# Kernel tuning notes

Measured on AMD Instinct MI355X. Metric: run time of the kernel, lower is better.

## Reference

```python
import jax, jax.numpy as jnp
import numpy as np

NEG_INF = -1e9


def setup_inputs() -> dict:
    key0 = jax.random.key(0)
    ks = jax.random.split(key0, 7)
    B, Tq, Tv, D, U = 8, 512, 512, 512, 128
    query = jax.random.normal(ks[0], (B, Tq, D), dtype=jnp.float32)
    key = jax.random.normal(ks[1], (B, Tv, D), dtype=jnp.float32)
    value = jax.random.normal(ks[2], (B, Tv, D), dtype=jnp.float32)
    mask = jax.random.randint(ks[3], (B, Tv), 0, 2).astype(bool)
    mask = mask.at[:, 0].set(True)  # ensure no fully-masked row
    Wa = jax.random.normal(ks[4], (D, U), dtype=jnp.float32) * (1.0 / np.sqrt(D))
    Ua = jax.random.normal(ks[5], (D, U), dtype=jnp.float32) * (1.0 / np.sqrt(D))
    scale = jax.random.normal(ks[6], (U,), dtype=jnp.float32) * 0.1
    return {"query": query, "key": key, "value": value, "mask": mask,
            "Wa": Wa, "Ua": Ua, "scale": scale}


def reference(query, key, value, mask, Wa, Ua, scale):
    # Dense projections (no bias)
    q = query @ Wa          # [B, Tq, U]
    k = key @ Ua            # [B, Tv, U]
    # Additive (Bahdanau) scores with learned per-unit scale:
    # scores[b,i,j] = sum_u scale[u] * tanh(q[b,i,u] + k[b,j,u])
    t = jnp.tanh(q[:, :, None, :] + k[:, None, :, :])   # [B, Tq, Tv, U]
    scores = jnp.einsum('bijU,U->bij', t, scale)         # [B, Tq, Tv]
    # Mask padded keys/values then softmax over Tv
    scores = jnp.where(mask[:, None, :], scores, NEG_INF)
    weights = jax.nn.softmax(scores, axis=-1)            # [B, Tq, Tv]
    # Weighted sum of values (query_mask is all-True in source -> no-op)
    context = jnp.einsum('bij,bjd->bid', weights, value) # [B, Tq, D]
    return context
```

## Files before the change

### kernel.cpp

```cpp
#include <hip/hip_runtime.h>

constexpr int Bb = 8;
constexpr int Tq = 512;
constexpr int Tv = 512;
constexpr int Dd = 512;
constexpr int Uu = 128;
constexpr float C2LOG2E = 2.88539008177792681f;
constexpr float LOG2E   = 1.44269504088896341f;

__global__ __launch_bounds__(256, 4) void proj_kernel(
    const float* __restrict__ query,
    const float* __restrict__ key,
    const float* __restrict__ Wa,
    const float* __restrict__ Ua,
    const int* __restrict__ mask,
    float* __restrict__ qf2, float* __restrict__ kT)
{
    const int R    = blockIdx.x * 8;
    const bool isQ = R < Bb * Tq;
    const float* __restrict__ src = isQ ? query : key;
    const float* __restrict__ W   = isQ ? Wa : Ua;
    const int Rloc = isQ ? R : R - Bb * Tq;

    __shared__ float x[8 * Dd];
    __shared__ int posLoc[8];
    const int t = threadIdx.x;

    {
        const float4* __restrict__ s4 =
            reinterpret_cast<const float4*>(src + (size_t)Rloc * Dd);
        float4* x4 = reinterpret_cast<float4*>(x);
#pragma unroll
        for (int m = 0; m < 4; ++m) x4[t + 256 * m] = s4[t + 256 * m];
    }
    if (!isQ && t < 64) {
        const int b  = Rloc >> 9;
        const int j0 = Rloc & 511;
        int base = 0;
#pragma unroll
        for (int c = 0; c < 8; ++c) {
            const int j = c * 64 + t;
            const int v = (mask[b * 512 + j] != 0);
            const unsigned long long bits = __ballot(v);
            const int pos = base + (int)__popcll(bits & ((1ull << t) - 1ull));
            if (j >= j0 && j < j0 + 8) posLoc[j - j0] = v ? pos : -1;
            base += (int)__popcll(bits);
        }
    }
    __syncthreads();

    const int ub = t & 63;
    const int dq = t >> 6;
    const float* __restrict__ Wq = W + (size_t)dq * 128 * Uu;
    const float* __restrict__ xq = x + dq * 128;

    float acc[8][2];
#pragma unroll
    for (int r = 0; r < 8; ++r) { acc[r][0] = 0.f; acc[r][1] = 0.f; }

#pragma unroll 2
    for (int d4 = 0; d4 < 32; ++d4) {
        const int d = d4 * 4;
        const float w0x = Wq[(d + 0) * Uu + ub], w1x = Wq[(d + 0) * Uu + ub + 64];
        const float w0y = Wq[(d + 1) * Uu + ub], w1y = Wq[(d + 1) * Uu + ub + 64];
        const float w0z = Wq[(d + 2) * Uu + ub], w1z = Wq[(d + 2) * Uu + ub + 64];
        const float w0w = Wq[(d + 3) * Uu + ub], w1w = Wq[(d + 3) * Uu + ub + 64];
#pragma unroll
        for (int r = 0; r < 8; ++r) {
            const float4 xv = *reinterpret_cast<const float4*>(xq + r * Dd + d);
            acc[r][0] = fmaf(xv.x, w0x, acc[r][0]);
            acc[r][0] = fmaf(xv.y, w0y, acc[r][0]);
            acc[r][0] = fmaf(xv.z, w0z, acc[r][0]);
            acc[r][0] = fmaf(xv.w, w0w, acc[r][0]);
            acc[r][1] = fmaf(xv.x, w1x, acc[r][1]);
            acc[r][1] = fmaf(xv.y, w1y, acc[r][1]);
            acc[r][1] = fmaf(xv.z, w1z, acc[r][1]);
            acc[r][1] = fmaf(xv.w, w1w, acc[r][1]);
        }
    }

    __syncthreads();
    {
        float* __restrict__ part = x;
#pragma unroll
        for (int r = 0; r < 8; ++r) {
            part[(dq * 8 + r) * 128 + ub]      = acc[r][0];
            part[(dq * 8 + r) * 128 + ub + 64] = acc[r][1];
        }
    }
    __syncthreads();

    {
        const float* __restrict__ part = x;
        const int r  = t >> 5;
        const int u0 = (t & 31) * 4;
        const float4 p0 = *reinterpret_cast<const float4*>(part + (0 * 8 + r) * 128 + u0);
        const float4 p1 = *reinterpret_cast<const float4*>(part + (1 * 8 + r) * 128 + u0);
        const float4 p2 = *reinterpret_cast<const float4*>(part + (2 * 8 + r) * 128 + u0);
        const float4 p3 = *reinterpret_cast<const float4*>(part + (3 * 8 + r) * 128 + u0);
        float4 v;
        v.x = C2LOG2E * (p0.x + p1.x + p2.x + p3.x);
        v.y = C2LOG2E * (p0.y + p1.y + p2.y + p3.y);
        v.z = C2LOG2E * (p0.z + p1.z + p2.z + p3.z);
        v.w = C2LOG2E * (p0.w + p1.w + p2.w + p3.w);
        if (isQ) {
            *reinterpret_cast<float4*>(qf2 + (size_t)(Rloc + r) * Uu + u0) = v;
        } else {
            const int p = posLoc[r];
            if (p >= 0) {
                float* __restrict__ kb = kT + (size_t)(Rloc >> 9) * Uu * Tv;
                const int u4a = u0 >> 2;
                *reinterpret_cast<float4*>(kb + ((size_t)u4a * Tv + p) * 4) = v;
            }
        }
    }
}

__global__ __launch_bounds__(512, 8) void attn_kernel(
    const float* __restrict__ qf2, const float* __restrict__ kT,
    const float* __restrict__ value,
    const int* __restrict__ mask,
    const float* __restrict__ scale,
    float* __restrict__ out)
{
    const int bid = blockIdx.x;
    const int swz = (bid & 7) * 128 + (bid >> 3);
    const int r0 = swz * 4;
    const int b  = r0 >> 9;
    const int t  = threadIdx.x;

    __shared__ float q2[4 * Uu];
    __shared__ float s2[Uu];
    __shared__ int   jl[Tv];
    __shared__ float w[4 * Tv];
    __shared__ float pbuf[4 * Tv];
    __shared__ float inv4[4];
    __shared__ int   cntS;

    jl[t] = 0;
    if (t < 128)
        reinterpret_cast<float4*>(q2)[t] =
            reinterpret_cast<const float4*>(qf2 + (size_t)r0 * Uu)[t];
    else if (t < 256) s2[t - 128] = scale[t - 128];
    __syncthreads();
    if (t < 64) {
        int base = 0;
#pragma unroll
        for (int c = 0; c < 8; ++c) {
            const int j = c * 64 + t;
            const int v = (mask[b * 512 + j] != 0);
            const unsigned long long bits = __ballot(v);
            const int pos = base + (int)__popcll(bits & ((1ull << t) - 1ull));
            if (v) jl[pos] = j;
            base += (int)__popcll(bits);
        }
        if (t == 0) cntS = base;
    }
    __syncthreads();

    const int cnt   = cntS;
    const int cntp4 = (cnt + 3) & ~3;

    {
        const int g   = t >> 8;
        const int jc0 = t & 255;
        const float4* __restrict__ kb4 =
            reinterpret_cast<const float4*>(kT) + (size_t)b * 32 * Tv + (size_t)g * 16 * Tv;
        float* __restrict__ wr = g ? pbuf : w;
        for (int jb = 0; jb < cnt; jb += 256) {
            const int jc = jb + jc0;
            if (jc < cnt) {
                float acc[4] = {0, 0, 0, 0};
#pragma unroll 2
                for (int u4 = 0; u4 < 16; ++u4) {
                    const float4 kv = kb4[(size_t)u4 * Tv + jc];
                    const float4 sv = reinterpret_cast<const float4*>(s2)[g * 16 + u4];
#pragma unroll
                    for (int i = 0; i < 4; ++i) {
                        const float4 qv = *reinterpret_cast<const float4*>(
                            q2 + i * Uu + (g * 16 + u4) * 4);
                        float e0 = __builtin_amdgcn_exp2f(qv.x + kv.x);
                        float e1 = __builtin_amdgcn_exp2f(qv.y + kv.y);
                        float e2 = __builtin_amdgcn_exp2f(qv.z + kv.z);
                        float e3 = __builtin_amdgcn_exp2f(qv.w + kv.w);
                        acc[i] = fmaf(sv.x, __builtin_amdgcn_rcpf(e0 + 1.f), acc[i]);
                        acc[i] = fmaf(sv.y, __builtin_amdgcn_rcpf(e1 + 1.f), acc[i]);
                        acc[i] = fmaf(sv.z, __builtin_amdgcn_rcpf(e2 + 1.f), acc[i]);
                        acc[i] = fmaf(sv.w, __builtin_amdgcn_rcpf(e3 + 1.f), acc[i]);
                    }
                }
#pragma unroll
                for (int i = 0; i < 4; ++i) wr[i * Tv + jc] = acc[i];
            }
        }
    }
    __syncthreads();

    {
        const int wv = t >> 6, ln = t & 63;
        if (wv < 4) {
            float* __restrict__ row        = w    + wv * Tv;
            const float* __restrict__ rowB = pbuf + wv * Tv;
            float vals[8];
            float m = -3e38f;
#pragma unroll
            for (int c = 0; c < 8; ++c) {
                const int e = ln + 64 * c;
                vals[c] = (e < cnt) ? -2.f * (row[e] + rowB[e]) : -3e38f;
                m = fmaxf(m, vals[c]);
            }
#pragma unroll
            for (int off = 32; off; off >>= 1) m = fmaxf(m, __shfl_xor(m, off, 64));
            float sum = 0.f;
#pragma unroll
            for (int c = 0; c < 8; ++c) {
                const int e = ln + 64 * c;
                if (e < cnt) {
                    float ex = __builtin_amdgcn_exp2f((vals[c] - m) * LOG2E);
                    row[e] = ex;
                    sum += ex;
                } else {
                    row[e] = 0.f;
                }
            }
#pragma unroll
            for (int off = 32; off; off >>= 1) sum += __shfl_xor(sum, off, 64);
            if (ln == 0) inv4[wv] = 1.0f / sum;
        }
    }
    __syncthreads();

    const int mid = ((cntp4 >> 1) + 3) & ~3;
    const int g  = t >> 8;
    const int c  = t & 255;
    const int d0 = c * 2;
    const int jbeg = g ? mid : 0;
    const int jend = g ? cntp4 : mid;
    const float* __restrict__ vb = value + (size_t)b * Tv * Dd + d0;
    float ax[4], ay[4];
#pragma unroll
    for (int i = 0; i < 4; ++i) { ax[i] = 0.f; ay[i] = 0.f; }

    for (int jj = jbeg; jj < jend; jj += 4) {
        const int4 rows = *reinterpret_cast<const int4*>(jl + jj);
        const float2 v0 = *reinterpret_cast<const float2*>(vb + (size_t)rows.x * Dd);
        const float2 v1 = *reinterpret_cast<const float2*>(vb + (size_t)rows.y * Dd);
        const float2 v2 = *reinterpret_cast<const float2*>(vb + (size_t)rows.z * Dd);
        const float2 v3 = *reinterpret_cast<const float2*>(vb + (size_t)rows.w * Dd);
#pragma unroll
        for (int i = 0; i < 4; ++i) {
            const float4 wq = *reinterpret_cast<const float4*>(w + i * Tv + jj);
            ax[i] = fmaf(wq.x, v0.x, ax[i]); ay[i] = fmaf(wq.x, v0.y, ay[i]);
            ax[i] = fmaf(wq.y, v1.x, ax[i]); ay[i] = fmaf(wq.y, v1.y, ay[i]);
            ax[i] = fmaf(wq.z, v2.x, ax[i]); ay[i] = fmaf(wq.z, v2.y, ay[i]);
            ax[i] = fmaf(wq.w, v3.x, ax[i]); ay[i] = fmaf(wq.w, v3.y, ay[i]);
        }
    }

    if (g == 1) {
#pragma unroll
        for (int i = 0; i < 4; ++i) {
            float2 p; p.x = ax[i]; p.y = ay[i];
            *reinterpret_cast<float2*>(pbuf + i * Dd + d0) = p;
        }
    }
    __syncthreads();
    if (g == 0) {
#pragma unroll
        for (int i = 0; i < 4; ++i) {
            const float inv = inv4[i];
            const float2 p1 = *reinterpret_cast<const float2*>(pbuf + i * Dd + d0);
            float2 o;
            o.x = (ax[i] + p1.x) * inv;
            o.y = (ay[i] + p1.y) * inv;
            *reinterpret_cast<float2*>(out + (size_t)(r0 + i) * Dd + d0) = o;
        }
    }
}

extern "C" void kernel_launch(void* const* d_in, const int* in_sizes, int n_in,
                              void* d_out, int out_size, void* d_ws, size_t ws_size,
                              hipStream_t stream)
{
    const float* query = (const float*)d_in[0];
    const float* key   = (const float*)d_in[1];
    const float* value = (const float*)d_in[2];
    const int*   mask  = (const int*)d_in[3];
    const float* Wa    = (const float*)d_in[4];
    const float* Ua    = (const float*)d_in[5];
    const float* scale = (const float*)d_in[6];
    float* out = (float*)d_out;

    float* qf2 = (float*)d_ws;
    float* kT  = qf2 + Bb * Tq * Uu;

    proj_kernel<<<(2 * Bb * Tq) / 8, 256, 0, stream>>>(query, key, Wa, Ua, mask, qf2, kT);
    attn_kernel<<<(Bb * Tq) / 4, 512, 0, stream>>>(qf2, kT, value, mask, scale, out);
}
```

Before: 153.5 us.

## Precompute exponentials in projection so attention uses product instead of exp

The projection kernel now stores exp2(2*log2e*q) and exp2(2*log2e*k) instead of the scaled projections. The attention inner loop then forms 1 + eq*ek with one FMA in place of an exp2 of a sum, cutting a transcendental from the hot Tv*U*Tq loop. The projection is also reorganised to 512 threads, each covering 64 of the D dimensions, with an 8-way partial reduction. Risk: exp of large projections can overflow to inf or lose precision, though rcp(inf) still gives 0 so tanh saturation stays correct.

Measured after the change: 151.2 us. Within noise of the previous version (-1.5%).

```diff
diff --git a/kernel.cpp b/kernel.cpp
--- a/kernel.cpp
+++ b/kernel.cpp
@@ -8,7 +8,7 @@
 constexpr float C2LOG2E = 2.88539008177792681f;
 constexpr float LOG2E   = 1.44269504088896341f;
 
-__global__ __launch_bounds__(256, 4) void proj_kernel(
+__global__ __launch_bounds__(512, 8) void proj_kernel(
     const float* __restrict__ query,
     const float* __restrict__ key,
     const float* __restrict__ Wa,
@@ -22,8 +22,9 @@
     const float* __restrict__ W   = isQ ? Wa : Ua;
     const int Rloc = isQ ? R : R - Bb * Tq;
 
-    __shared__ float x[8 * Dd];
+    __shared__ float smem[8 * 8 * 128];
     __shared__ int posLoc[8];
+    float* __restrict__ x = smem;
     const int t = threadIdx.x;
 
     {
@@ -31,7 +32,7 @@
             reinterpret_cast<const float4*>(src + (size_t)Rloc * Dd);
         float4* x4 = reinterpret_cast<float4*>(x);
 #pragma unroll
-        for (int m = 0; m < 4; ++m) x4[t + 256 * m] = s4[t + 256 * m];
+        for (int m = 0; m < 2; ++m) x4[t + 512 * m] = s4[t + 512 * m];
     }
     if (!isQ && t < 64) {
         const int b  = Rloc >> 9;
@@ -51,15 +52,15 @@
 
     const int ub = t & 63;
     const int dq = t >> 6;
-    const float* __restrict__ Wq = W + (size_t)dq * 128 * Uu;
-    const float* __restrict__ xq = x + dq * 128;
+    const float* __restrict__ Wq = W + (size_t)dq * 64 * Uu;
+    const float* __restrict__ xq = x + dq * 64;
 
     float acc[8][2];
 #pragma unroll
     for (int r = 0; r < 8; ++r) { acc[r][0] = 0.f; acc[r][1] = 0.f; }
 
 #pragma unroll 2
-    for (int d4 = 0; d4 < 32; ++d4) {
+    for (int d4 = 0; d4 < 16; ++d4) {
         const int d = d4 * 4;
         const float w0x = Wq[(d + 0) * Uu + ub], w1x = Wq[(d + 0) * Uu + ub + 64];
         const float w0y = Wq[(d + 1) * Uu + ub], w1y = Wq[(d + 1) * Uu + ub + 64];
@@ -81,7 +82,7 @@
 
     __syncthreads();
     {
-        float* __restrict__ part = x;
+        float* __restrict__ part = smem;
 #pragma unroll
         for (int r = 0; r < 8; ++r) {
             part[(dq * 8 + r) * 128 + ub]      = acc[r][0];
@@ -91,26 +92,28 @@
     __syncthreads();
 
     {
-        const float* __restrict__ part = x;
-        const int r  = t >> 5;
-        const int u0 = (t & 31) * 4;
-        const float4 p0 = *reinterpret_cast<const float4*>(part + (0 * 8 + r) * 128 + u0);
-        const float4 p1 = *reinterpret_cast<const float4*>(part + (1 * 8 + r) * 128 + u0);
-        const float4 p2 = *reinterpret_cast<const float4*>(part + (2 * 8 + r) * 128 + u0);
-        const float4 p3 = *reinterpret_cast<const float4*>(part + (3 * 8 + r) * 128 + u0);
-        float4 v;
-        v.x = C2LOG2E * (p0.x + p1.x + p2.x + p3.x);
-        v.y = C2LOG2E * (p0.y + p1.y + p2.y + p3.y);
-        v.z = C2LOG2E * (p0.z + p1.z + p2.z + p3.z);
-        v.w = C2LOG2E * (p0.w + p1.w + p2.w + p3.w);
+        const float* __restrict__ part = smem;
+        const int r  = t >> 6;
+        const int u0 = (t & 63) * 2;
+        float s0 = 0.f, s1 = 0.f;
+#pragma unroll
+        for (int p = 0; p < 8; ++p) {
+            const float2 pv = *reinterpret_cast<const float2*>(part + (p * 8 + r) * 128 + u0);
+            s0 += pv.x;
+            s1 += pv.y;
+        }
+        float2 e;
+        e.x = __builtin_amdgcn_exp2f(C2LOG2E * s0);
+        e.y = __builtin_amdgcn_exp2f(C2LOG2E * s1);
         if (isQ) {
-            *reinterpret_cast<float4*>(qf2 + (size_t)(Rloc + r) * Uu + u0) = v;
+            *reinterpret_cast<float2*>(qf2 + (size_t)(Rloc + r) * Uu + u0) = e;
         } else {
             const int p = posLoc[r];
             if (p >= 0) {
                 float* __restrict__ kb = kT + (size_t)(Rloc >> 9) * Uu * Tv;
-                const int u4a = u0 >> 2;
-                *reinterpret_cast<float4*>(kb + ((size_t)u4a * Tv + p) * 4) = v;
+                const int u4 = u0 >> 2;
+                const int c  = u0 & 3;
+                *reinterpret_cast<float2*>(kb + ((size_t)u4 * Tv + p) * 4 + c) = e;
             }
         }
     }
@@ -179,14 +182,14 @@
                     for (int i = 0; i < 4; ++i) {
                         const float4 qv = *reinterpret_cast<const float4*>(
                             q2 + i * Uu + (g * 16 + u4) * 4);
-                        float e0 = __builtin_amdgcn_exp2f(qv.x + kv.x);
-                        float e1 = __builtin_amdgcn_exp2f(qv.y + kv.y);
-                        float e2 = __builtin_amdgcn_exp2f(qv.z + kv.z);
-                        float e3 = __builtin_amdgcn_exp2f(qv.w + kv.w);
-                        acc[i] = fmaf(sv.x, __builtin_amdgcn_rcpf(e0 + 1.f), acc[i]);
-                        acc[i] = fmaf(sv.y, __builtin_amdgcn_rcpf(e1 + 1.f), acc[i]);
-                        acc[i] = fmaf(sv.z, __builtin_amdgcn_rcpf(e2 + 1.f), acc[i]);
-                        acc[i] = fmaf(sv.w, __builtin_amdgcn_rcpf(e3 + 1.f), acc[i]);
+                        const float p0 = fmaf(qv.x, kv.x, 1.f);
+                        const float p1 = fmaf(qv.y, kv.y, 1.f);
+                        const float p2 = fmaf(qv.z, kv.z, 1.f);
+                        const float p3 = fmaf(qv.w, kv.w, 1.f);
+                        acc[i] = fmaf(sv.x, __builtin_amdgcn_rcpf(p0), acc[i]);
+                        acc[i] = fmaf(sv.y, __builtin_amdgcn_rcpf(p1), acc[i]);
+                        acc[i] = fmaf(sv.z, __builtin_amdgcn_rcpf(p2), acc[i]);
+                        acc[i] = fmaf(sv.w, __builtin_amdgcn_rcpf(p3), acc[i]);
                     }
                 }
 #pragma unroll
@@ -294,6 +297,6 @@
     float* qf2 = (float*)d_ws;
     float* kT  = qf2 + Bb * Tq * Uu;
 
-    proj_kernel<<<(2 * Bb * Tq) / 8, 256, 0, stream>>>(query, key, Wa, Ua, mask, qf2, kT);
+    proj_kernel<<<(2 * Bb * Tq) / 8, 512, 0, stream>>>(query, key, Wa, Ua, mask, qf2, kT);
     attn_kernel<<<(Bb * Tq) / 4, 512, 0, stream>>>(qf2, kT, value, mask, scale, out);
 }
```
